# Kernel optimization log

Measured on AMD Instinct MI355X. Metric: run time of the kernel, lower is better.

## Reference

```python
import jax, jax.numpy as jnp
import numpy as np

INPUT_DIM = 1024
HIDDEN_DIM = 64   # per-head dim
NUM_HEADS = 16
PROJ = HIDDEN_DIM * NUM_HEADS  # 1024


def setup_inputs() -> dict:
    key = jax.random.key(0)
    ks = jax.random.split(key, 9)
    s = 1.0 / np.sqrt(INPUT_DIM)
    x = jax.random.normal(ks[0], (4, 2048, INPUT_DIM), dtype=jnp.float32)
    # Linear weights stored [in, out] (math-equivalent to torch's W.T)
    Wq = jax.random.uniform(ks[1], (INPUT_DIM, PROJ), jnp.float32, -s, s)
    bq = jax.random.uniform(ks[2], (PROJ,), jnp.float32, -s, s)
    Wk = jax.random.uniform(ks[3], (INPUT_DIM, PROJ), jnp.float32, -s, s)
    bk = jax.random.uniform(ks[4], (PROJ,), jnp.float32, -s, s)
    Wv = jax.random.uniform(ks[5], (INPUT_DIM, PROJ), jnp.float32, -s, s)
    bv = jax.random.uniform(ks[6], (PROJ,), jnp.float32, -s, s)
    sf = 1.0 / np.sqrt(PROJ)
    Wf = jax.random.uniform(ks[7], (PROJ, HIDDEN_DIM), jnp.float32, -sf, sf)
    bf = jax.random.uniform(ks[8], (HIDDEN_DIM,), jnp.float32, -sf, sf)
    return {"x": x, "Wq": Wq, "bq": bq, "Wk": Wk, "bk": bk,
            "Wv": Wv, "bv": bv, "Wf": Wf, "bf": bf}


def reference(x, Wq, bq, Wk, bk, Wv, bv, Wf, bf):
    B, S, _ = x.shape
    def split_heads(t):  # [B,S,H*D] -> [B,H,S,D]
        return t.reshape(B, S, NUM_HEADS, HIDDEN_DIM).transpose(0, 2, 1, 3)
    q = split_heads(x @ Wq + bq)
    k = split_heads(x @ Wk + bk)
    v = split_heads(x @ Wv + bv)
    scale = 1.0 / jnp.sqrt(jnp.float32(HIDDEN_DIM))
    scores = jnp.einsum('bhqd,bhkd->bhqk', q, k) * scale  # [B,H,S,S]
    weights = jax.nn.softmax(scores, axis=-1)
    ctx = jnp.einsum('bhqk,bhkd->bhqd', weights, v)
    ctx = ctx.transpose(0, 2, 1, 3).reshape(B, S, PROJ)
    return ctx @ Wf + bf  # [B,S,HIDDEN_DIM]
```

## Files before the change

kernel.cpp:

```cpp
#include <hip/hip_runtime.h>
#include <math.h>

#define S_LEN 2048
#define NH 16
#define HD 64
#define DMODEL 1024
#define BATCH 4
#define M_TOT (BATCH * S_LEN)

typedef __attribute__((ext_vector_type(8))) short bf16x8;
typedef __attribute__((ext_vector_type(4))) float f32x4;

#define CK 0.18033688f

__device__ __forceinline__ unsigned short f2bf_rne(float f) {
    unsigned u = __float_as_uint(f);
    u += 0x7fffu + ((u >> 16) & 1u);
    return (unsigned short)(u >> 16);
}

__device__ __forceinline__ void gld16(unsigned short* lds, const unsigned short* g) {
    __builtin_amdgcn_global_load_lds(
        (const __attribute__((address_space(1))) void*)g,
        (__attribute__((address_space(3))) void*)lds, 16, 0, 0);
}

__global__ __launch_bounds__(256) void cvt_fused(
    const float* __restrict__ x,
    const float* __restrict__ Wq, const float* __restrict__ Wk,
    const float* __restrict__ Wv, const float* __restrict__ Wf,
    unsigned short* __restrict__ xb, unsigned short* __restrict__ WT)
{
    const int z = blockIdx.z;
    const int tid = threadIdx.x;

    if (z < 4) {
        if (z == 3 && blockIdx.x > 0) return;
        const float* W = (z == 0) ? Wq : (z == 1) ? Wk : (z == 2) ? Wv : Wf;
        const int ncol = (z == 3) ? 64 : DMODEL;
        unsigned short* out = WT + (size_t)z * DMODEL * DMODEL;

        __shared__ float Lt[64][65];
        const int r0 = blockIdx.y * 64;
        const int c0 = blockIdx.x * 64;

        #pragma unroll
        for (int p = 0; p < 4; p++) {
            int row = (tid >> 4) + p * 16;
            int c4 = (tid & 15) * 4;
            float4 v = *(const float4*)(W + (size_t)(r0 + row) * ncol + c0 + c4);
            Lt[row][c4 + 0] = v.x; Lt[row][c4 + 1] = v.y;
            Lt[row][c4 + 2] = v.z; Lt[row][c4 + 3] = v.w;
        }
        __syncthreads();
        #pragma unroll
        for (int p = 0; p < 4; p++) {
            int nr = (tid >> 4) + p * 16;
            int kc = (tid & 15) * 4;
            unsigned short t[4];
            #pragma unroll
            for (int j = 0; j < 4; j++) t[j] = f2bf_rne(Lt[kc + j][nr]);
            *(uint2*)(out + (size_t)(c0 + nr) * DMODEL + r0 + kc) = *(uint2*)t;
        }
    } else {
        const int gtid = (blockIdx.y * 16 + blockIdx.x) * 256 + tid;
        #pragma unroll
        for (int it = 0; it < 8; it++) {
            #pragma unroll
            for (int k = 0; k < 4; k++) {
                size_t i = ((size_t)((it * 4 + k) * 65536) + gtid) * 4;
                float4 v = *(const float4*)(x + i);
                unsigned short t[4];
                t[0] = f2bf_rne(v.x); t[1] = f2bf_rne(v.y);
                t[2] = f2bf_rne(v.z); t[3] = f2bf_rne(v.w);
                *(uint2*)(xb + i) = *(uint2*)t;
            }
        }
    }
}

__global__ __launch_bounds__(512) void qkv_fused_mfma(
    const unsigned short* __restrict__ xb,
    const unsigned short* __restrict__ WT,
    const float* __restrict__ bq, const float* __restrict__ bk,
    const float* __restrict__ bv,
    unsigned short* __restrict__ Qb, unsigned short* __restrict__ Kb,
    unsigned short* __restrict__ Vtb)
{
    __shared__ __align__(16) unsigned short Ws[2][24 * 512];
    __shared__ __align__(16) unsigned short Bs[2][32 * 512];

    const int lin = blockIdx.x;
    const int xcd = lin & 7;
    const int s   = lin >> 3;
    const int rb  = xcd * 4 + (s & 3);
    const int ocb = s >> 2;

    const int tid = threadIdx.x;
    const int lane = tid & 63, w = tid >> 6;
    const int quad = lane >> 4, l15 = lane & 15;

    const int R0  = rb * 256;
    const int OC0 = ocb * 64;

    const unsigned short* gW0 = WT +
        (size_t)(OC0 + (w >> 1) * 16 + l15) * DMODEL + (w & 1) * 32 + quad * 8;
    const unsigned short* gW1 = gW0 + (size_t)DMODEL * DMODEL;
    const unsigned short* gW2 = gW1 + (size_t)DMODEL * DMODEL;
    const unsigned short* gB0 = xb + (size_t)(R0 + w * 16 + l15) * DMODEL + quad * 8;
    const unsigned short* gB1 = gB0 + (size_t)128 * DMODEL;

    f32x4 acc[3][4][2];
    #pragma unroll
    for (int z = 0; z < 3; z++)
        #pragma unroll
        for (int i = 0; i < 4; i++)
            #pragma unroll
            for (int j = 0; j < 2; j++)
                #pragma unroll
                for (int c = 0; c < 4; c++) acc[z][i][j][c] = 0.f;

#define QKV_STAGE(BUF, K)  do {                                        \
        gld16(Ws[BUF] + (0 * 8 + w) * 512, gW0 + (K));                 \
        gld16(Ws[BUF] + (1 * 8 + w) * 512, gW1 + (K));                 \
        gld16(Ws[BUF] + (2 * 8 + w) * 512, gW2 + (K));                 \
        gld16(Bs[BUF] + ((w + 0) * 2 + 0) * 512, gB0 + (K));           \
        gld16(Bs[BUF] + ((w + 0) * 2 + 1) * 512, gB0 + (K) + 32);      \
        gld16(Bs[BUF] + ((w + 8) * 2 + 0) * 512, gB1 + (K));           \
        gld16(Bs[BUF] + ((w + 8) * 2 + 1) * 512, gB1 + (K) + 32);      \
    } while (0)

    QKV_STAGE(0, 0);

    for (int t = 0; t < 16; ++t) {
        const int cur = t & 1;
        __syncthreads();
        if (t < 15) {
            if (cur == 0) QKV_STAGE(1, (t + 1) * 64);
            else          QKV_STAGE(0, (t + 1) * 64);
        }

        const unsigned short* Wb = Ws[cur];
        const unsigned short* Bb = Bs[cur];

        #pragma unroll
        for (int sl = 0; sl < 2; sl++) {
            bf16x8 bfr[2];
            #pragma unroll
            for (int j = 0; j < 2; j++)
                bfr[j] = *(const bf16x8*)&Bb[((2 * w + j) * 2 + sl) * 512 + lane * 8];
            #pragma unroll
            for (int z = 0; z < 3; z++) {
                bf16x8 af[4];
                #pragma unroll
                for (int i = 0; i < 4; i++)
                    af[i] = *(const bf16x8*)&Wb[(z * 8 + i * 2 + sl) * 512 + lane * 8];
                if (z != 2) {
                    #pragma unroll
                    for (int i = 0; i < 4; i++)
                        #pragma unroll
                        for (int j = 0; j < 2; j++)
                            acc[z][i][j] = __builtin_amdgcn_mfma_f32_16x16x32_bf16(
                                af[i], bfr[j], acc[z][i][j], 0, 0, 0);
                } else {
                    #pragma unroll
                    for (int i = 0; i < 4; i++)
                        #pragma unroll
                        for (int j = 0; j < 2; j++)
                            acc[2][i][j] = __builtin_amdgcn_mfma_f32_16x16x32_bf16(
                                bfr[j], af[i], acc[2][i][j], 0, 0, 0);
                }
            }
        }
    }
#undef QKV_STAGE

    #pragma unroll
    for (int z = 0; z < 2; z++) {
        unsigned short* out = (z == 0) ? Qb : Kb;
        const float* bias = (z == 0) ? bq : bk;
        const float qs = (z == 0) ? CK : 1.0f;
        #pragma unroll
        for (int i = 0; i < 4; i++) {
            int oc = OC0 + i * 16 + quad * 4;
            float4 bv4 = *(const float4*)&bias[oc];
            #pragma unroll
            for (int j = 0; j < 2; j++) {
                int row = R0 + w * 32 + j * 16 + l15;
                unsigned short t4[4];
                t4[0] = f2bf_rne((acc[z][i][j][0] + bv4.x) * qs);
                t4[1] = f2bf_rne((acc[z][i][j][1] + bv4.y) * qs);
                t4[2] = f2bf_rne((acc[z][i][j][2] + bv4.z) * qs);
                t4[3] = f2bf_rne((acc[z][i][j][3] + bv4.w) * qs);
                *(uint2*)(out + (size_t)row * DMODEL + oc) = *(uint2*)t4;
            }
        }
    }
    {
        const int b = R0 >> 11;
        const int sbase = (R0 & 2047) + w * 32;
        #pragma unroll
        for (int i = 0; i < 4; i++) {
            int oc = OC0 + i * 16 + l15;
            float bvv = bv[oc];
            #pragma unroll
            for (int j = 0; j < 2; j++) {
                int sq = sbase + j * 16 + quad * 4;
                unsigned short t4[4];
                t4[0] = f2bf_rne(acc[2][i][j][0] + bvv);
                t4[1] = f2bf_rne(acc[2][i][j][1] + bvv);
                t4[2] = f2bf_rne(acc[2][i][j][2] + bvv);
                t4[3] = f2bf_rne(acc[2][i][j][3] + bvv);
                *(uint2*)(Vtb + (size_t)(b * DMODEL + oc) * S_LEN + sq) = *(uint2*)t4;
            }
        }
    }
}

__global__ __launch_bounds__(256, 4) void flash_attn_mfma(
    const unsigned short* __restrict__ Qg,
    const unsigned short* __restrict__ Kg,
    const unsigned short* __restrict__ Vtg,
    unsigned short* __restrict__ ctxb)
{
    __shared__ __align__(16) unsigned short Ks[16 * 512];
    __shared__ __align__(16) unsigned short Vs[16 * 512];
    __shared__ __align__(16) unsigned short Ps[8 * 512];

    const int tid  = threadIdx.x;
    const int lane = tid & 63, w = tid >> 6;
    const int quad = lane >> 4, l15 = lane & 15;

    const int lin = blockIdx.x + 16 * (blockIdx.y + 16 * blockIdx.z);
    const int xcd = lin & 7;
    const int s   = lin >> 3;
    const int bh  = xcd + 8 * (s >> 4);
    const int qblk = s & 15;
    const int b = bh >> 4, h = bh & 15;
    const int r0 = qblk * 128;

    bf16x8 qf[2][2];
    #pragma unroll
    for (int nt = 0; nt < 2; nt++)
        #pragma unroll
        for (int ds = 0; ds < 2; ds++)
            qf[nt][ds] = *(const bf16x8*)(Qg +
                (size_t)(b * S_LEN + r0 + w * 32 + nt * 16 + l15) * DMODEL +
                h * HD + ds * 32 + quad * 8);

    const unsigned short* gK = Kg + (size_t)(b * S_LEN + w * 16 + l15) * DMODEL + h * HD + quad * 8;
    const unsigned short* gV = Vtg + ((size_t)((b * NH + h) * HD + w * 16 + l15)) * S_LEN + quad * 8;

    f32x4 O[2][4], lsum[2];
    #pragma unroll
    for (int rt = 0; rt < 2; rt++) {
        #pragma unroll
        for (int c = 0; c < 4; c++) lsum[rt][c] = 0.f;
        #pragma unroll
        for (int dt = 0; dt < 4; dt++)
            #pragma unroll
            for (int c = 0; c < 4; c++) O[rt][dt][c] = 0.f;
    }

    f32x4 zero4;
    #pragma unroll
    for (int c = 0; c < 4; c++) zero4[c] = 0.f;
    bf16x8 ones;
    #pragma unroll
    for (int c = 0; c < 8; c++) ones[c] = (short)0x3F80;

    for (int st = 0; st < S_LEN / 128; st++) {
        __syncthreads();
        gld16(Ks + ((w + 0) * 2 + 0) * 512, gK);
        gld16(Ks + ((w + 0) * 2 + 1) * 512, gK + 32);
        gld16(Ks + ((w + 4) * 2 + 0) * 512, gK + (size_t)64 * DMODEL);
        gld16(Ks + ((w + 4) * 2 + 1) * 512, gK + (size_t)64 * DMODEL + 32);
        gld16(Vs + (w * 4 + 0) * 512, gV);
        gld16(Vs + (w * 4 + 1) * 512, gV + 32);
        gld16(Vs + (w * 4 + 2) * 512, gV + 64);
        gld16(Vs + (w * 4 + 3) * 512, gV + 96);
        gK += (size_t)128 * DMODEL;
        gV += 128;
        __syncthreads();

        #pragma unroll
        for (int r = 0; r < 4; r++) {
            f32x4 sc[2][2];
            {
                bf16x8 kf0 = *(const bf16x8*)&Ks[((r * 2 + 0) * 2 + 0) * 512 + lane * 8];
                bf16x8 kf1 = *(const bf16x8*)&Ks[((r * 2 + 1) * 2 + 0) * 512 + lane * 8];
                sc[0][0] = __builtin_amdgcn_mfma_f32_16x16x32_bf16(kf0, qf[0][0], zero4, 0, 0, 0);
                sc[0][1] = __builtin_amdgcn_mfma_f32_16x16x32_bf16(kf0, qf[1][0], zero4, 0, 0, 0);
                sc[1][0] = __builtin_amdgcn_mfma_f32_16x16x32_bf16(kf1, qf[0][0], zero4, 0, 0, 0);
                sc[1][1] = __builtin_amdgcn_mfma_f32_16x16x32_bf16(kf1, qf[1][0], zero4, 0, 0, 0);
                kf0 = *(const bf16x8*)&Ks[((r * 2 + 0) * 2 + 1) * 512 + lane * 8];
                kf1 = *(const bf16x8*)&Ks[((r * 2 + 1) * 2 + 1) * 512 + lane * 8];
                sc[0][0] = __builtin_amdgcn_mfma_f32_16x16x32_bf16(kf0, qf[0][1], sc[0][0], 0, 0, 0);
                sc[0][1] = __builtin_amdgcn_mfma_f32_16x16x32_bf16(kf0, qf[1][1], sc[0][1], 0, 0, 0);
                sc[1][0] = __builtin_amdgcn_mfma_f32_16x16x32_bf16(kf1, qf[0][1], sc[1][0], 0, 0, 0);
                sc[1][1] = __builtin_amdgcn_mfma_f32_16x16x32_bf16(kf1, qf[1][1], sc[1][1], 0, 0, 0);
            }

            #pragma unroll
            for (int nt = 0; nt < 2; nt++) {
                #pragma unroll
                for (int mt = 0; mt < 2; mt++) {
                    unsigned u[4];
                    #pragma unroll
                    for (int c = 0; c < 4; c++)
                        u[c] = __float_as_uint(__builtin_amdgcn_exp2f(sc[mt][nt][c]));
                    uint2 pk;
                    pk.x = __builtin_amdgcn_perm(u[1], u[0], 0x07060302u);
                    pk.y = __builtin_amdgcn_perm(u[3], u[2], 0x07060302u);
                    int off = (w * 2 + nt) * 512 + (mt * 2 + (quad >> 1)) * 128 +
                              l15 * 8 + (quad & 1) * 4;
                    *(uint2*)&Ps[off] = pk;
                }
            }

            bf16x8 pf0 = *(const bf16x8*)&Ps[(w * 2 + 0) * 512 + lane * 8];
            bf16x8 pf1 = *(const bf16x8*)&Ps[(w * 2 + 1) * 512 + lane * 8];
            lsum[0] = __builtin_amdgcn_mfma_f32_16x16x32_bf16(pf0, ones, lsum[0], 0, 0, 0);
            lsum[1] = __builtin_amdgcn_mfma_f32_16x16x32_bf16(pf1, ones, lsum[1], 0, 0, 0);
            #pragma unroll
            for (int dt = 0; dt < 4; dt++) {
                bf16x8 vf = *(const bf16x8*)&Vs[(dt * 4 + r) * 512 + lane * 8];
                O[0][dt] = __builtin_amdgcn_mfma_f32_16x16x32_bf16(pf0, vf, O[0][dt], 0, 0, 0);
                O[1][dt] = __builtin_amdgcn_mfma_f32_16x16x32_bf16(pf1, vf, O[1][dt], 0, 0, 0);
            }
        }
    }

    const size_t srow = (size_t)(b * S_LEN + r0 + w * 32);
    #pragma unroll
    for (int rt = 0; rt < 2; rt++) {
        #pragma unroll
        for (int reg = 0; reg < 4; reg++) {
            float li = 1.0f / lsum[rt][reg];
            size_t rowoff = (srow + rt * 16 + quad * 4 + reg) * DMODEL + h * HD + l15;
            #pragma unroll
            for (int dt = 0; dt < 4; dt++)
                ctxb[rowoff + dt * 16] = f2bf_rne(O[rt][dt][reg] * li);
        }
    }
}

__global__ __launch_bounds__(512) void out_proj_mfma(
    const unsigned short* __restrict__ ctxb,
    const unsigned short* __restrict__ WfT,
    const float* __restrict__ bfb,
    float* __restrict__ out)
{
    __shared__ float Red[8 * 1024];

    const int tid = threadIdx.x;
    const int lane = tid & 63, w = tid >> 6;
    const int quad = lane >> 4, l15 = lane & 15;
    const int m0 = blockIdx.x * 16;

    const unsigned short* pA = ctxb + (size_t)(m0 + l15) * DMODEL + w * 128 + quad * 8;
    const unsigned short* pB = WfT + (size_t)l15 * DMODEL + w * 128 + quad * 8;

    f32x4 acc[4];
    #pragma unroll
    for (int j = 0; j < 4; j++)
        #pragma unroll
        for (int c = 0; c < 4; c++) acc[j][c] = 0.f;

    #pragma unroll
    for (int k0 = 0; k0 < 128; k0 += 32) {
        bf16x8 af = *(const bf16x8*)(pA + k0);
        #pragma unroll
        for (int j = 0; j < 4; j++) {
            bf16x8 bfr = *(const bf16x8*)(pB + (size_t)j * 16 * DMODEL + k0);
            acc[j] = __builtin_amdgcn_mfma_f32_16x16x32_bf16(af, bfr, acc[j], 0, 0, 0);
        }
    }

    #pragma unroll
    for (int j = 0; j < 4; j++)
        #pragma unroll
        for (int reg = 0; reg < 4; reg++)
            Red[w * 1024 + lane * 16 + j * 4 + reg] = acc[j][reg];
    __syncthreads();

    const int row = tid >> 5;
    const int c0  = (tid & 31) * 2;
    float2 o;
    float* op = &o.x;
    #pragma unroll
    for (int cc = 0; cc < 2; cc++) {
        int col = c0 + cc;
        int idx = ((row >> 2) * 16 + (col & 15)) * 16 + (col >> 4) * 4 + (row & 3);
        float s = 0.f;
        #pragma unroll
        for (int wv = 0; wv < 8; wv++) s += Red[wv * 1024 + idx];
        op[cc] = s + bfb[col];
    }
    *(float2*)(out + (size_t)(m0 + row) * HD + c0) = o;
}

extern "C" void kernel_launch(void* const* d_in, const int* in_sizes, int n_in,
                              void* d_out, int out_size, void* d_ws, size_t ws_size,
                              hipStream_t stream)
{
    (void)in_sizes; (void)n_in; (void)out_size; (void)ws_size;
    const float* x  = (const float*)d_in[0];
    const float* Wq = (const float*)d_in[1];
    const float* bq = (const float*)d_in[2];
    const float* Wk = (const float*)d_in[3];
    const float* bk = (const float*)d_in[4];
    const float* Wv = (const float*)d_in[5];
    const float* bv = (const float*)d_in[6];
    const float* Wf = (const float*)d_in[7];
    const float* bf = (const float*)d_in[8];
    float* out = (float*)d_out;

    char* wsb = (char*)d_ws;
    unsigned short* xb   = (unsigned short*)wsb;
    unsigned short* ctxb = (unsigned short*)wsb;
    unsigned short* WT   = xb + (size_t)M_TOT * DMODEL;
    unsigned short* WfT  = WT + (size_t)3 * DMODEL * DMODEL;
    unsigned short* Qb   = (unsigned short*)(wsb + (size_t)32 * 1024 * 1024);
    unsigned short* Kb   = Qb + (size_t)M_TOT * DMODEL;
    unsigned short* Vtb  = Kb + (size_t)M_TOT * DMODEL;

    cvt_fused<<<dim3(16, 16, 5), 256, 0, stream>>>(x, Wq, Wk, Wv, Wf, xb, WT);
    qkv_fused_mfma<<<dim3(512), 512, 0, stream>>>(xb, WT, bq, bk, bv, Qb, Kb, Vtb);
    flash_attn_mfma<<<dim3(S_LEN / 128, NH, BATCH), 256, 0, stream>>>(Qb, Kb, Vtb, ctxb);
    out_proj_mfma<<<dim3(M_TOT / 16), 512, 0, stream>>>(ctxb, WfT, bf, out);
}
```

Measured before the change: 268.6 us.

## Double flash-attention query tile to 256 rows with 8-wave blocks

Each attention block now processes 256 query rows with 8 waves instead of 128 rows with 4, so each K/V tile loaded into LDS is shared by twice as many queries. This halves the K/V global traffic per query. Loading is also split so waves 0-3 fetch K and waves 4-7 fetch V. The P staging buffer is doubled and the grid is flattened to 512 blocks with an XCD-aware mapping. In exchange the grid has half as many blocks, LDS use per block rises, and the K tile layout written to LDS changes, which must match the unseen compute loop.

```diff
diff --git a/kernel.cpp b/kernel.cpp
--- a/kernel.cpp
+++ b/kernel.cpp
@@ -217,7 +217,7 @@
     }
 }
 
-__global__ __launch_bounds__(256, 4) void flash_attn_mfma(
+__global__ __launch_bounds__(512, 4) void flash_attn_mfma(
     const unsigned short* __restrict__ Qg,
     const unsigned short* __restrict__ Kg,
     const unsigned short* __restrict__ Vtg,
@@ -225,19 +225,19 @@
 {
     __shared__ __align__(16) unsigned short Ks[16 * 512];
     __shared__ __align__(16) unsigned short Vs[16 * 512];
-    __shared__ __align__(16) unsigned short Ps[8 * 512];
+    __shared__ __align__(16) unsigned short Ps[16 * 512];
 
     const int tid  = threadIdx.x;
     const int lane = tid & 63, w = tid >> 6;
     const int quad = lane >> 4, l15 = lane & 15;
 
-    const int lin = blockIdx.x + 16 * (blockIdx.y + 16 * blockIdx.z);
+    const int lin = blockIdx.x;
     const int xcd = lin & 7;
     const int s   = lin >> 3;
-    const int bh  = xcd + 8 * (s >> 4);
-    const int qblk = s & 15;
+    const int bh  = xcd + 8 * (s >> 3);
+    const int qblk = s & 7;
     const int b = bh >> 4, h = bh & 15;
-    const int r0 = qblk * 128;
+    const int r0 = qblk * 256;
 
     bf16x8 qf[2][2];
     #pragma unroll
@@ -248,8 +248,11 @@
                 (size_t)(b * S_LEN + r0 + w * 32 + nt * 16 + l15) * DMODEL +
                 h * HD + ds * 32 + quad * 8);
 
-    const unsigned short* gK = Kg + (size_t)(b * S_LEN + w * 16 + l15) * DMODEL + h * HD + quad * 8;
-    const unsigned short* gV = Vtg + ((size_t)((b * NH + h) * HD + w * 16 + l15)) * S_LEN + quad * 8;
+    const int sw = w & 3;
+    const unsigned short* gK = Kg +
+        (size_t)(b * S_LEN + sw * 32 + l15) * DMODEL + h * HD + quad * 8;
+    const unsigned short* gV = Vtg +
+        ((size_t)(bh * HD + sw * 16 + l15)) * S_LEN + quad * 8;
 
     f32x4 O[2][4], lsum[2];
     #pragma unroll
@@ -271,16 +274,19 @@
 
     for (int st = 0; st < S_LEN / 128; st++) {
         __syncthreads();
-        gld16(Ks + ((w + 0) * 2 + 0) * 512, gK);
-        gld16(Ks + ((w + 0) * 2 + 1) * 512, gK + 32);
-        gld16(Ks + ((w + 4) * 2 + 0) * 512, gK + (size_t)64 * DMODEL);
-        gld16(Ks + ((w + 4) * 2 + 1) * 512, gK + (size_t)64 * DMODEL + 32);
-        gld16(Vs + (w * 4 + 0) * 512, gV);
-        gld16(Vs + (w * 4 + 1) * 512, gV + 32);
-        gld16(Vs + (w * 4 + 2) * 512, gV + 64);
-        gld16(Vs + (w * 4 + 3) * 512, gV + 96);
-        gK += (size_t)128 * DMODEL;
-        gV += 128;
+        if (w < 4) {
+            gld16(Ks + (w * 4 + 0) * 512, gK);
+            gld16(Ks + (w * 4 + 1) * 512, gK + 32);
+            gld16(Ks + (w * 4 + 2) * 512, gK + (size_t)16 * DMODEL);
+            gld16(Ks + (w * 4 + 3) * 512, gK + (size_t)16 * DMODEL + 32);
+            gK += (size_t)128 * DMODEL;
+        } else {
+            gld16(Vs + (sw * 4 + 0) * 512, gV);
+            gld16(Vs + (sw * 4 + 1) * 512, gV + 32);
+            gld16(Vs + (sw * 4 + 2) * 512, gV + 64);
+            gld16(Vs + (sw * 4 + 3) * 512, gV + 96);
+            gV += 128;
+        }
         __syncthreads();
 
         #pragma unroll
@@ -427,6 +433,6 @@
 
     cvt_fused<<<dim3(16, 16, 5), 256, 0, stream>>>(x, Wq, Wk, Wv, Wf, xb, WT);
     qkv_fused_mfma<<<dim3(512), 512, 0, stream>>>(xb, WT, bq, bk, bv, Qb, Kb, Vtb);
-    flash_attn_mfma<<<dim3(S_LEN / 128, NH, BATCH), 256, 0, stream>>>(Qb, Kb, Vtb, ctxb);
+    flash_attn_mfma<<<dim3(512), 512, 0, stream>>>(Qb, Kb, Vtb, ctxb);
     out_proj_mfma<<<dim3(M_TOT / 16), 512, 0, stream>>>(ctxb, WfT, bf, out);
 }
```

Result: faster. 257.3 us (-4.2%).
